# Performance work log

Hardware: AMD Instinct MI355X
Metric: run time of the kernel (lower is better)

The kernel has to match this reference:

```python
import jax, jax.numpy as jnp
import numpy as np

PARENTS = [-1, 0, 0, 0, 1, 2, 3, 4, 5, 6, 7, 8, 9, 9, 9, 12, 13, 14, 16, 17, 18, 19, 20, 21]
K = 24          # num_joints (SMPL kinematic tree)
BONE = 12       # 3x3 rotation (9) + 3 rel offset
FEAT = 64       # local_feature_size
B = 65536       # batch
NIN = BONE + 1 + FEAT  # 77: bone_transform(13) concat parent feature(64)


def setup_inputs() -> dict:
    key = jax.random.key(0)
    ks = jax.random.split(key, 6)
    pose = jax.random.normal(ks[0], (B, K, 3, 3), jnp.float32)
    rel_joints = jax.random.normal(ks[1], (B, K, 3), jnp.float32)
    # proj_bone_prior: Linear(K*BONE -> FEAT)
    Wp = jax.random.normal(ks[2], (K * BONE, FEAT), jnp.float32) * 0.05
    bp = jnp.zeros((FEAT,), jnp.float32)
    # per-joint BoneMLP: Linear(NIN->NIN), ReLU, Linear(NIN->FEAT), ReLU (stacked over K)
    W1 = jax.random.normal(ks[3], (K, NIN, NIN), jnp.float32) * 0.05
    b1 = jnp.zeros((K, NIN), jnp.float32)
    W2 = jax.random.normal(ks[4], (K, NIN, FEAT), jnp.float32) * 0.05
    b2 = jnp.zeros((K, FEAT), jnp.float32)
    return {"pose": pose, "rel_joints": rel_joints, "Wp": Wp, "bp": bp,
            "W1": W1, "b1": b1, "W2": W2, "b2": b2}


def reference(pose, rel_joints, Wp, bp, W1, b1, W2, b2):
    Bn, Kn = rel_joints.shape[0], rel_joints.shape[1]
    bone_lengths = jnp.linalg.norm(rel_joints, axis=-1, keepdims=True)          # B,K,1
    bone_features = jnp.concatenate([pose.reshape(Bn, Kn, 9), rel_joints], -1)  # B,K,12
    root_bone_prior = bone_features.reshape(Bn, -1) @ Wp + bp                   # B,FEAT
    bone_transforms = jnp.concatenate([bone_features, bone_lengths], -1)        # B,K,13
    feats = [None] * Kn
    for i in range(Kn):  # fixed structural loop over kinematic tree (K=24)
        parent = PARENTS[i]
        pf = root_bone_prior if parent == -1 else feats[parent]
        x = jnp.concatenate([bone_transforms[:, i, :], pf], axis=-1)  # B,77
        h = jax.nn.relu(x @ W1[i] + b1[i])
        feats[i] = jax.nn.relu(h @ W2[i] + b2[i])
    return jnp.concatenate(feats, axis=-1)  # B, K*FEAT
```

## Files before the change

### kernel.cpp

```cpp
#include <hip/hip_runtime.h>
#include <hip/hip_bf16.h>
#include <math.h>

typedef __attribute__((ext_vector_type(8))) short short8;
typedef __attribute__((ext_vector_type(4))) float f32x4;

#define NJ 24

#define F1_J   7680
#define F2_OFF (NJ*F1_J)
#define F2_J   6144
#define FP_OFF (F2_OFF + NJ*F2_J)
#define IMG_SHORTS (FP_OFF + 36*512)

#define MFMA(A,B,C) __builtin_amdgcn_mfma_f32_16x16x32_bf16((A),(B),(C),0,0,0)

__constant__ int ORD[24] = {0,1,4,7,10, 2,5,8,11, 3,6,9, 12,15, 13,16,18,20,22, 14,17,19,21,23};
__constant__ int PSL[24] = {2,0,1,1,1,  0,1,1,1,  0,0,0,  0,1,   0,1,1,1,1,    0,0,0,0,0};
__constant__ int SSL[24] = {0,1,1,1,-1, 1,1,1,-1, 0,0,0,  1,-1,  1,1,1,1,-1,   0,0,0,0,-1};

__device__ __forceinline__ short f2bf(float f) {
  union { float f; unsigned u; } v; v.f = f;
  unsigned r = v.u + 0x7FFFu + ((v.u >> 16) & 1u);
  return (short)(r >> 16);
}
__device__ __forceinline__ short sbf(float f) {
  __hip_bfloat16 h = __float2bfloat16(f);
  return *reinterpret_cast<short*>(&h);
}
__device__ __forceinline__ short8 pk8(f32x4 lo, f32x4 hi) {
  union { short8 s; unsigned u[4]; } r;
  asm("v_cvt_pk_bf16_f32 %0, %1, %2" : "=v"(r.u[0]) : "v"(lo[0]), "v"(lo[1]));
  asm("v_cvt_pk_bf16_f32 %0, %1, %2" : "=v"(r.u[1]) : "v"(lo[2]), "v"(lo[3]));
  asm("v_cvt_pk_bf16_f32 %0, %1, %2" : "=v"(r.u[2]) : "v"(hi[0]), "v"(hi[1]));
  asm("v_cvt_pk_bf16_f32 %0, %1, %2" : "=v"(r.u[3]) : "v"(hi[2]), "v"(hi[3]));
  return r.s;
}

__global__ __launch_bounds__(256) void prep_kernel(
    const float* __restrict__ W1, const float* __restrict__ W2,
    const float* __restrict__ Wp, const float* __restrict__ b1,
    const float* __restrict__ b2, short* __restrict__ img) {
  int t = blockIdx.x * 256 + threadIdx.x;
  if (t >= IMG_SHORTS) return;
  float v = 0.f;
  if (t < F2_OFF) {
    int i = t / F1_J, r = t % F1_J;
    int blk = r >> 9, q = r & 511;
    int ln = q >> 3, e = q & 7;
    int nt = blk / 3, s = blk - nt*3;
    int n  = nt*16 + (ln & 15);
    int kp = s*32 + (ln >> 4)*8 + e;
    if (kp == 13) {
      v = (n < 77) ? b1[i*77 + n] : (n == 77 ? 1.f : 0.f);
    } else if (n < 77) {
      if (kp < 13)                  v = W1[i*5929 + kp*77 + n];
      else if (kp >= 16 && kp < 80) v = W1[i*5929 + (kp-3)*77 + n];
    }
  } else if (t < FP_OFF) {
    int u = t - F2_OFF;
    int i = u / F2_J, r = u % F2_J;
    int blk = r >> 9, q = r & 511;
    int ln = q >> 3, e = q & 7;
    int nt = blk / 3, s = blk - nt*3;
    int n  = nt*16 + (ln & 15);
    int k  = s*32 + (ln >> 4)*8 + e;
    if (k < 77)       v = W2[i*4928 + k*64 + n];
    else if (k == 77) v = b2[i*64 + n];
  } else {
    int u = t - FP_OFF;
    int blk = u >> 9, q = u & 511;
    int ln = q >> 3, e = q & 7;
    int nt = blk / 9, s = blk - nt*9;
    int n  = nt*16 + (ln & 15);
    int kp = s*32 + (ln >> 4)*8 + e;
    int j, w;
    if (kp < 216) { j = kp / 9;       w = kp % 9; }
    else          { j = (kp-216) / 3; w = 9 + (kp-216) % 3; }
    v = Wp[(j*12 + w)*64 + n];
  }
  img[t] = f2bf(v);
}

#define ISSUE_W1(JN) do { \
  unsigned long long _b = img_u + (unsigned long long)(JN)*15360ull; \
  asm volatile( \
    "global_load_dwordx4 %0, %15, %16\n"  "global_load_dwordx4 %1, %15, %16 offset:1024\n" \
    "global_load_dwordx4 %2, %15, %16 offset:2048\n" "global_load_dwordx4 %3, %15, %16 offset:3072\n" \
    "global_load_dwordx4 %4, %15, %17\n"  "global_load_dwordx4 %5, %15, %17 offset:1024\n" \
    "global_load_dwordx4 %6, %15, %17 offset:2048\n" "global_load_dwordx4 %7, %15, %17 offset:3072\n" \
    "global_load_dwordx4 %8, %15, %18\n"  "global_load_dwordx4 %9, %15, %18 offset:1024\n" \
    "global_load_dwordx4 %10, %15, %18 offset:2048\n" "global_load_dwordx4 %11, %15, %18 offset:3072\n" \
    "global_load_dwordx4 %12, %15, %19\n" "global_load_dwordx4 %13, %15, %19 offset:1024\n" \
    "global_load_dwordx4 %14, %15, %19 offset:2048\n" \
    : "=&v"(fw1[0]),"=&v"(fw1[1]),"=&v"(fw1[2]),"=&v"(fw1[3]),"=&v"(fw1[4]), \
      "=&v"(fw1[5]),"=&v"(fw1[6]),"=&v"(fw1[7]),"=&v"(fw1[8]),"=&v"(fw1[9]), \
      "=&v"(fw1[10]),"=&v"(fw1[11]),"=&v"(fw1[12]),"=&v"(fw1[13]),"=&v"(fw1[14]) \
    : "v"(voff), "s"(_b), "s"(_b+4096ull), "s"(_b+8192ull), "s"(_b+12288ull) \
    : "memory"); \
} while(0)

#define ISSUE_BTW2(J) do { \
  unsigned long long _b = img_u + 368640ull + (unsigned long long)(J)*12288ull; \
  asm volatile( \
    "global_load_dword %0, %20, off\n" \
    "global_load_dword %1, %20, off offset:4\n" \
    "global_load_dword %2, %20, off offset:8\n" \
    "global_load_dword %3, %20, off offset:12\n" \
    "global_load_dword %4, %21, %22\n" \
    "global_load_dword %5, %21, %22 offset:4\n" \
    "global_load_dword %6, %21, %22 offset:8\n" \
    "global_load_dword %7, %21, %22 offset:12\n" \
    "global_load_dwordx4 %8, %23, %24\n"  "global_load_dwordx4 %9, %23, %24 offset:1024\n" \
    "global_load_dwordx4 %10, %23, %24 offset:2048\n" "global_load_dwordx4 %11, %23, %24 offset:3072\n" \
    "global_load_dwordx4 %12, %23, %25\n" "global_load_dwordx4 %13, %23, %25 offset:1024\n" \
    "global_load_dwordx4 %14, %23, %25 offset:2048\n" "global_load_dwordx4 %15, %23, %25 offset:3072\n" \
    "global_load_dwordx4 %16, %23, %26\n" "global_load_dwordx4 %17, %23, %26 offset:1024\n" \
    "global_load_dwordx4 %18, %23, %26 offset:2048\n" "global_load_dwordx4 %19, %23, %26 offset:3072\n" \
    : "=&v"(d0),"=&v"(d1),"=&v"(d2),"=&v"(d3),"=&v"(d4),"=&v"(d5),"=&v"(d6),"=&v"(d7), \
      "=&v"(fw2[0]),"=&v"(fw2[1]),"=&v"(fw2[2]),"=&v"(fw2[3]),"=&v"(fw2[4]),"=&v"(fw2[5]), \
      "=&v"(fw2[6]),"=&v"(fw2[7]),"=&v"(fw2[8]),"=&v"(fw2[9]),"=&v"(fw2[10]),"=&v"(fw2[11]) \
    : "v"(aA), "v"(vB), "s"(pose_u), "v"(voff), \
      "s"(_b), "s"(_b+4096ull), "s"(_b+8192ull) \
    : "memory"); \
} while(0)

#define WAITV(N) do { asm volatile("s_waitcnt vmcnt(" #N ")" ::: "memory"); \
                      __builtin_amdgcn_sched_barrier(0); } while(0)

__global__ __launch_bounds__(256, 2) void enc_kernel(
    const float* __restrict__ pose, const float* __restrict__ rel,
    const float* __restrict__ bp,  const short* __restrict__ img,
    float* __restrict__ out) {
  __shared__ __align__(16) short lds[4*10240];

  const int tid  = threadIdx.x;
  const int lane = tid & 63;
  const int wv   = tid >> 6;
  short* myl   = lds + wv*10240;
  short* featL = myl;
  short* hL    = myl + 6912;
  short* btL   = myl + 9472;

  const int cl  = lane & 15;
  const int g   = lane >> 4;
  const int rw0 = blockIdx.x*128 + wv*32;
  const short8 zz = {0,0,0,0,0,0,0,0};
  const unsigned long long img_u  = (unsigned long long)img;
  const unsigned long long pose_u = (unsigned long long)pose;
  const unsigned long long rel_u  = (unsigned long long)rel;
  const unsigned voff = (unsigned)lane << 4;
  const int btr = lane >> 1, btq = lane & 1;
  const unsigned btProw = (unsigned)((rw0 + btr)*864);
  const unsigned btRrow = (unsigned)((rw0 + btr)*288);

  short8 fw1[15], fw2[12];
  float d0, d1, d2, d3, d4, d5, d6, d7;

  {
    const float* pb = pose + (size_t)(rw0 + btr)*216;
    const float* rb = rel  + (size_t)(rw0 + btr)*72;
    short8 w;
    if (btq == 0) {
      w = pk8(*(const f32x4*)pb, *(const f32x4*)(pb + 4));
    } else {
      float r0 = rb[0], r1 = rb[1], r2 = rb[2];
      float nv = sqrtf(r0*r0 + r1*r1 + r2*r2);
      w[0]=sbf(pb[8]); w[1]=sbf(r0); w[2]=sbf(r1); w[3]=sbf(r2);
      w[4]=sbf(nv); w[5]=(short)0x3F80; w[6]=0; w[7]=0;
    }
    *(short8*)(btL + btr*24 + btq*8) = w;
  }

  f32x4 racc[2][4] = {};
  {
    const float* pr0 = pose + (size_t)(rw0 + cl)*216;
    const float* rr0 = rel  + (size_t)(rw0 + cl)*72;
    const float* pr1 = pose + (size_t)(rw0 + 16 + cl)*216;
    const float* rr1 = rel  + (size_t)(rw0 + 16 + cl)*72;
    const short8* fpg = (const short8*)(img + FP_OFF) + lane;
    short8 av0[9], av1[9];
#pragma unroll
    for (int s = 0; s < 9; ++s) {
      int k0 = s*32 + g*8;
      const float* s0 = (k0 < 216) ? (pr0 + k0) : (rr0 + (k0 - 216));
      const float* s1 = (k0 < 216) ? (pr1 + k0) : (rr1 + (k0 - 216));
      av0[s] = pk8(*(const f32x4*)s0, *(const f32x4*)(s0 + 4));
      av1[s] = pk8(*(const f32x4*)s1, *(const f32x4*)(s1 + 4));
    }
#pragma unroll
    for (int nt = 0; nt < 4; ++nt) {
      short8 fwp[9];
#pragma unroll
      for (int s = 0; s < 9; ++s) fwp[s] = fpg[(nt*9 + s)*64];
#pragma unroll
      for (int s = 0; s < 9; ++s) {
        racc[0][nt] = MFMA(av0[s], fwp[s], racc[0][nt]);
        racc[1][nt] = MFMA(av1[s], fwp[s], racc[1][nt]);
      }
    }
  }
#pragma unroll
  for (int nt = 0; nt < 4; ++nt) {
    int n = nt*16 + cl;
    float bias = bp[n];
#pragma unroll
    for (int m = 0; m < 2; ++m)
#pragma unroll
      for (int r4 = 0; r4 < 4; ++r4)
        featL[2*2304 + (m*16 + g*4 + r4)*72 + n] = sbf(racc[m][nt][r4] + bias);
  }

  ISSUE_W1(0);

#pragma unroll 1
  for (int p = 0; p < NJ; ++p) {
    const int j  = ORD[p];
    const int ps = PSL[p];
    const int ss = SSL[p];
    const int jn = (p < NJ-1) ? ORD[p+1] : 0;

    const short* fb0 = featL + ps*2304 + cl*72;
    const short* fb1 = featL + ps*2304 + (16 + cl)*72;
    short8 a0[2], a1[2], a2[2];
    a0[0] = (g < 2) ? *(const short8*)(btL + cl*24 + g*8)
                    : *(const short8*)(fb0 + (g-2)*8);
    a0[1] = (g < 2) ? *(const short8*)(btL + (16+cl)*24 + g*8)
                    : *(const short8*)(fb1 + (g-2)*8);
    a1[0] = *(const short8*)(fb0 + 16 + g*8);
    a1[1] = *(const short8*)(fb1 + 16 + g*8);
    a2[0] = (g < 2) ? *(const short8*)(fb0 + 48 + g*8) : zz;
    a2[1] = (g < 2) ? *(const short8*)(fb1 + 48 + g*8) : zz;

    const unsigned long long aA =
        btq ? (rel_u  + btRrow + (unsigned)(jn ? jn*12 - 4 : 0))
            : (pose_u + btProw + (unsigned)(jn*36));
    const unsigned vB = btProw + (unsigned)(jn*36) + (btq ? 20u : 16u);
    ISSUE_BTW2(j);

    if (p == 0) { WAITV(20); } else { WAITV(52); }

#pragma unroll
    for (int nt = 0; nt < 5; ++nt) {
      f32x4 c0 = {0,0,0,0}, c1 = {0,0,0,0};
      c0 = MFMA(a0[0], fw1[nt*3+0], c0);  c1 = MFMA(a0[1], fw1[nt*3+0], c1);
      c0 = MFMA(a1[0], fw1[nt*3+1], c0);  c1 = MFMA(a1[1], fw1[nt*3+1], c1);
      c0 = MFMA(a2[0], fw1[nt*3+2], c0);  c1 = MFMA(a2[1], fw1[nt*3+2], c1);
      int n = nt*16 + cl;
#pragma unroll
      for (int r4 = 0; r4 < 4; ++r4) {
        hL[(g*4 + r4)*80 + n]      = sbf(fmaxf(c0[r4], 0.f));
        hL[(16 + g*4 + r4)*80 + n] = sbf(fmaxf(c1[r4], 0.f));
      }
    }
    short8 h0[2], h1[2], h2[2];
#pragma unroll
    for (int m = 0; m < 2; ++m) {
      const short* hb = hL + (m*16 + cl)*80;
      h0[m] = *(const short8*)(hb + g*8);
      h1[m] = *(const short8*)(hb + 32 + g*8);
      h2[m] = (g < 2) ? *(const short8*)(hb + 64 + g*8) : zz;
    }

    ISSUE_W1(jn);
    WAITV(15);

    {
      f32x4 lo = {d0, d1, d2, d3}, hi = {d4, d5, d6, d7};
      short8 wA = pk8(lo, hi);
      float r0 = jn ? d1 : d0;
      float r1 = jn ? d2 : d1;
      float r2 = jn ? d3 : d2;
      float nv = sqrtf(r0*r0 + r1*r1 + r2*r2);
      short8 wB;
      wB[0]=sbf(d7);   wB[1]=sbf(r0); wB[2]=sbf(r1); wB[3]=sbf(r2);
      wB[4]=sbf(nv); wB[5]=(short)0x3F80; wB[6]=0; wB[7]=0;
      short8 w = btq ? wB : wA;
      *(short8*)(btL + btr*24 + btq*8) = w;
    }

#pragma unroll
    for (int nt = 0; nt < 4; ++nt) {
      f32x4 c0 = {0,0,0,0}, c1 = {0,0,0,0};
      c0 = MFMA(h0[0], fw2[nt*3+0], c0);  c1 = MFMA(h0[1], fw2[nt*3+0], c1);
      c0 = MFMA(h1[0], fw2[nt*3+1], c0);  c1 = MFMA(h1[1], fw2[nt*3+1], c1);
      c0 = MFMA(h2[0], fw2[nt*3+2], c0);  c1 = MFMA(h2[1], fw2[nt*3+2], c1);
      int n = nt*16 + cl;
#pragma unroll
      for (int m = 0; m < 2; ++m) {
        f32x4& cc = m ? c1 : c0;
        float* outb = out + (size_t)(rw0 + m*16 + g*4)*1536 + (size_t)j*64;
#pragma unroll
        for (int r4 = 0; r4 < 4; ++r4) {
          float v = fmaxf(cc[r4], 0.f);
          __builtin_nontemporal_store(v, &outb[(size_t)r4*1536 + n]);
          if (ss >= 0) featL[ss*2304 + (m*16 + g*4 + r4)*72 + n] = sbf(v);
        }
      }
    }
  }
}

extern "C" void kernel_launch(void* const* d_in, const int* in_sizes, int n_in,
                              void* d_out, int out_size, void* d_ws, size_t ws_size,
                              hipStream_t stream) {
  const float* pose = (const float*)d_in[0];
  const float* rel  = (const float*)d_in[1];
  const float* Wp   = (const float*)d_in[2];
  const float* bp   = (const float*)d_in[3];
  const float* W1   = (const float*)d_in[4];
  const float* b1   = (const float*)d_in[5];
  const float* W2   = (const float*)d_in[6];
  const float* b2   = (const float*)d_in[7];
  float* outp = (float*)d_out;
  short* img  = (short*)d_ws;
  const int Bn = in_sizes[0] / 216;
  prep_kernel<<<(IMG_SHORTS + 255)/256, 256, 0, stream>>>(W1, W2, Wp, b1, b2, img);
  enc_kernel<<<Bn/128, 256, 0, stream>>>(pose, rel, bp, img, outp);
}
```

Before: 154.4 us.

## Swap MFMA operands to transpose outputs for vectorized stores

Swaps the A/B operands of every MFMA so each lane holds four consecutive output columns of one row instead of four rows of one column. This allows 4-wide packed bf16 LDS writes and 16-byte nontemporal global stores instead of scalar ones, and the bias is loaded as a vector. The vmcnt wait threshold is lowered to match the reduced number of outstanding store instructions. A wrong wait count could create a race on outstanding loads.

```diff
diff --git a/kernel.cpp b/kernel.cpp
--- a/kernel.cpp
+++ b/kernel.cpp
@@ -3,6 +3,7 @@
 #include <math.h>
 
 typedef __attribute__((ext_vector_type(8))) short short8;
+typedef __attribute__((ext_vector_type(4))) short s4;
 typedef __attribute__((ext_vector_type(4))) float f32x4;
 
 #define NJ 24
@@ -35,6 +36,16 @@
   asm("v_cvt_pk_bf16_f32 %0, %1, %2" : "=v"(r.u[2]) : "v"(hi[0]), "v"(hi[1]));
   asm("v_cvt_pk_bf16_f32 %0, %1, %2" : "=v"(r.u[3]) : "v"(hi[2]), "v"(hi[3]));
   return r.s;
+}
+__device__ __forceinline__ s4 pk4(f32x4 v) {
+  union { s4 s; unsigned u[2]; } r;
+  asm("v_cvt_pk_bf16_f32 %0, %1, %2" : "=v"(r.u[0]) : "v"(v[0]), "v"(v[1]));
+  asm("v_cvt_pk_bf16_f32 %0, %1, %2" : "=v"(r.u[1]) : "v"(v[2]), "v"(v[3]));
+  return r.s;
+}
+__device__ __forceinline__ f32x4 relu4(f32x4 v) {
+  f32x4 r; r[0]=fmaxf(v[0],0.f); r[1]=fmaxf(v[1],0.f);
+  r[2]=fmaxf(v[2],0.f); r[3]=fmaxf(v[3],0.f); return r;
 }
 
 __global__ __launch_bounds__(256) void prep_kernel(
@@ -171,6 +182,9 @@
     }
     *(short8*)(btL + btr*24 + btq*8) = w;
   }
+  f32x4 bpv[4];
+#pragma unroll
+  for (int nt = 0; nt < 4; ++nt) bpv[nt] = *(const f32x4*)(bp + nt*16 + g*4);
 
   f32x4 racc[2][4] = {};
   {
@@ -195,20 +209,19 @@
       for (int s = 0; s < 9; ++s) fwp[s] = fpg[(nt*9 + s)*64];
 #pragma unroll
       for (int s = 0; s < 9; ++s) {
-        racc[0][nt] = MFMA(av0[s], fwp[s], racc[0][nt]);
-        racc[1][nt] = MFMA(av1[s], fwp[s], racc[1][nt]);
+        racc[0][nt] = MFMA(fwp[s], av0[s], racc[0][nt]);
+        racc[1][nt] = MFMA(fwp[s], av1[s], racc[1][nt]);
       }
     }
   }
 #pragma unroll
   for (int nt = 0; nt < 4; ++nt) {
-    int n = nt*16 + cl;
-    float bias = bp[n];
-#pragma unroll
-    for (int m = 0; m < 2; ++m)
-#pragma unroll
-      for (int r4 = 0; r4 < 4; ++r4)
-        featL[2*2304 + (m*16 + g*4 + r4)*72 + n] = sbf(racc[m][nt][r4] + bias);
+#pragma unroll
+    for (int m = 0; m < 2; ++m) {
+      f32x4 v = racc[m][nt];
+      v[0]+=bpv[nt][0]; v[1]+=bpv[nt][1]; v[2]+=bpv[nt][2]; v[3]+=bpv[nt][3];
+      *(s4*)(featL + 2*2304 + (m*16 + cl)*72 + nt*16 + g*4) = pk4(v);
+    }
   }
 
   ISSUE_W1(0);
@@ -238,20 +251,16 @@
     const unsigned vB = btProw + (unsigned)(jn*36) + (btq ? 20u : 16u);
     ISSUE_BTW2(j);
 
-    if (p == 0) { WAITV(20); } else { WAITV(52); }
+    if (p == 0) { WAITV(20); } else { WAITV(28); }
 
 #pragma unroll
     for (int nt = 0; nt < 5; ++nt) {
       f32x4 c0 = {0,0,0,0}, c1 = {0,0,0,0};
-      c0 = MFMA(a0[0], fw1[nt*3+0], c0);  c1 = MFMA(a0[1], fw1[nt*3+0], c1);
-      c0 = MFMA(a1[0], fw1[nt*3+1], c0);  c1 = MFMA(a1[1], fw1[nt*3+1], c1);
-      c0 = MFMA(a2[0], fw1[nt*3+2], c0);  c1 = MFMA(a2[1], fw1[nt*3+2], c1);
-      int n = nt*16 + cl;
-#pragma unroll
-      for (int r4 = 0; r4 < 4; ++r4) {
-        hL[(g*4 + r4)*80 + n]      = sbf(fmaxf(c0[r4], 0.f));
-        hL[(16 + g*4 + r4)*80 + n] = sbf(fmaxf(c1[r4], 0.f));
-      }
+      c0 = MFMA(fw1[nt*3+0], a0[0], c0);  c1 = MFMA(fw1[nt*3+0], a0[1], c1);
+      c0 = MFMA(fw1[nt*3+1], a1[0], c0);  c1 = MFMA(fw1[nt*3+1], a1[1], c1);
+      c0 = MFMA(fw1[nt*3+2], a2[0], c0);  c1 = MFMA(fw1[nt*3+2], a2[1], c1);
+      *(s4*)(hL + cl*80 + nt*16 + g*4)        = pk4(relu4(c0));
+      *(s4*)(hL + (16 + cl)*80 + nt*16 + g*4) = pk4(relu4(c1));
     }
     short8 h0[2], h1[2], h2[2];
 #pragma unroll
@@ -282,20 +291,17 @@
 #pragma unroll
     for (int nt = 0; nt < 4; ++nt) {
       f32x4 c0 = {0,0,0,0}, c1 = {0,0,0,0};
-      c0 = MFMA(h0[0], fw2[nt*3+0], c0);  c1 = MFMA(h0[1], fw2[nt*3+0], c1);
-      c0 = MFMA(h1[0], fw2[nt*3+1], c0);  c1 = MFMA(h1[1], fw2[nt*3+1], c1);
-      c0 = MFMA(h2[0], fw2[nt*3+2], c0);  c1 = MFMA(h2[1], fw2[nt*3+2], c1);
-      int n = nt*16 + cl;
-#pragma unroll
-      for (int m = 0; m < 2; ++m) {
-        f32x4& cc = m ? c1 : c0;
-        float* outb = out + (size_t)(rw0 + m*16 + g*4)*1536 + (size_t)j*64;
-#pragma unroll
-        for (int r4 = 0; r4 < 4; ++r4) {
-          float v = fmaxf(cc[r4], 0.f);
-          __builtin_nontemporal_store(v, &outb[(size_t)r4*1536 + n]);
-          if (ss >= 0) featL[ss*2304 + (m*16 + g*4 + r4)*72 + n] = sbf(v);
-        }
+      c0 = MFMA(fw2[nt*3+0], h0[0], c0);  c1 = MFMA(fw2[nt*3+0], h0[1], c1);
+      c0 = MFMA(fw2[nt*3+1], h1[0], c0);  c1 = MFMA(fw2[nt*3+1], h1[1], c1);
+      c0 = MFMA(fw2[nt*3+2], h2[0], c0);  c1 = MFMA(fw2[nt*3+2], h2[1], c1);
+      f32x4 v0 = relu4(c0), v1 = relu4(c1);
+      float* o0 = out + (size_t)(rw0 + cl)*1536      + (size_t)j*64 + nt*16 + g*4;
+      float* o1 = out + (size_t)(rw0 + 16 + cl)*1536 + (size_t)j*64 + nt*16 + g*4;
+      __builtin_nontemporal_store(v0, (f32x4*)o0);
+      __builtin_nontemporal_store(v1, (f32x4*)o1);
+      if (ss >= 0) {
+        *(s4*)(featL + ss*2304 + cl*72 + nt*16 + g*4)        = pk4(v0);
+        *(s4*)(featL + ss*2304 + (16 + cl)*72 + nt*16 + g*4) = pk4(v1);
       }
     }
   }
```

Measured after the change: 153.4 us. No clear change (-0.6%).
